# Kernel optimization log

Hardware: AMD Instinct MI355X
Metric: run time of the kernel (lower is better)

The kernel has to match this reference:

```python
import jax, jax.numpy as jnp
import numpy as np

SF, RES, TS = 8192, 40, 1  # sample freq, resolution (orders), time span (s)


def _eofft(inputs, rpm):
    """Engine-order FFT: per-sample zero-pad to length n_i = L + floor((RES*60/rpm_i - TS)*SF),
    FFT along time, keep first SF bins, take magnitude. Implemented as a fully batched
    Bluestein (chirp-z) transform so every sample uses the SAME fixed FFT size M,
    despite different logical FFT lengths n_i.
    """
    B, L, C = inputs.shape            # L == SF (required by the original .view)
    N = SF * TS                       # nonzero signal length after truncation (8192)
    K = SF                            # number of output bins kept (8192)
    M = int(2 ** np.ceil(np.log2(N + K - 1)))  # 16384, fixed batched FFT size

    x = inputs[:, :N, :]              # truncate, [B, N, C]
    pad = jnp.floor((RES * 60.0 / rpm - TS) * SF).astype(jnp.int32)  # [B]
    n = L + pad                       # per-sample DFT length n_i, [B] int32

    # Phases use exact integer m^2 mod 2n (exp(i*pi*q/n) has period 2n in q),
    # so float32 stays accurate even for large m.
    two_n = (2 * n)[:, None]                              # [B,1]
    nf = n.astype(jnp.float32)[:, None]                   # [B,1]

    # a[t] = x[t] * exp(-i*pi*t^2/n)
    t = jnp.arange(N, dtype=jnp.int32)
    a_phase = jnp.pi * ((t * t) % two_n).astype(jnp.float32) / nf      # [B,N]
    a = x.astype(jnp.complex64) * jnp.exp(-1j * a_phase)[:, :, None]   # [B,N,C]
    a = jnp.pad(a, ((0, 0), (0, M - N), (0, 0)))                       # [B,M,C]

    # b[m] = exp(+i*pi*m^2/n), laid out circularly: index m for m<K, index M-m for m=1..N-1
    m = jnp.arange(M, dtype=jnp.int32)
    mm = jnp.minimum(m, M - m)
    b_phase = jnp.pi * ((mm * mm) % two_n).astype(jnp.float32) / nf    # [B,M]
    b = jnp.exp(1j * b_phase)                                          # [B,M]

    # circular convolution via fixed-size FFTs (batched over B and C)
    conv = jnp.fft.ifft(jnp.fft.fft(a, axis=1) * jnp.fft.fft(b, axis=1)[:, :, None], axis=1)

    # X[k] = exp(-i*pi*k^2/n) * conv[k], k = 0..K-1
    k = jnp.arange(K, dtype=jnp.int32)
    k_phase = jnp.pi * ((k * k) % two_n).astype(jnp.float32) / nf      # [B,K]
    X = jnp.exp(-1j * k_phase)[:, :, None] * conv[:, :K, :]            # [B,K,C]
    return jnp.abs(X)                                                  # [B,SF,C] float32


def setup_inputs() -> dict:
    key = jax.random.key(0)
    k1, k2 = jax.random.split(key)
    B, L, C = 64, 8192, 8
    inputs = jax.random.normal(k1, (B, L, C), dtype=jnp.float32)
    rpm = jax.random.uniform(k2, (B,), dtype=jnp.float32, minval=600.0, maxval=2400.0)
    return {"inputs": inputs, "rpm": rpm}


def reference(inputs, rpm):
    return _eofft(inputs, rpm)
```

## Files before the change

kernel.cpp:

```cpp
#include <hip/hip_runtime.h>
#include <hip/hip_fp16.h>
#include <math.h>


static constexpr int Bn = 64;

#define PI_F 3.14159265358979323846f
#define TWO_PI_F 6.28318530717958647692f
#define R2_F 0.70710678118654752f

__device__ __forceinline__ int compute_n(float rpm) {
    return 8192 + (int)floorf((2400.0f / rpm - 1.0f) * 8192.0f);
}
__device__ __forceinline__ float2 cmul(float2 a, float2 b) {
    return make_float2(a.x*b.x - a.y*b.y, a.x*b.y + a.y*b.x);
}
__device__ __forceinline__ float2 cadd(float2 a, float2 b){ return make_float2(a.x+b.x, a.y+b.y); }
__device__ __forceinline__ float2 csub(float2 a, float2 b){ return make_float2(a.x-b.x, a.y-b.y); }
__device__ __forceinline__ float2 shflx1(float2 v) {
    return make_float2(__shfl_xor(v.x, 1, 64), __shfl_xor(v.y, 1, 64));
}
__device__ __forceinline__ int brev7(int x) { return (int)(__brev((unsigned)x) >> 25); }

__device__ __forceinline__ float f2h_bits(float2 a) {
    union { __half2 h; float f; } u;
    u.h = __float22half2_rn(a);
    return u.f;
}
__device__ __forceinline__ float2 h2f_bits(float w) {
    union { float f; __half2 h; } u;
    u.f = w;
    return __half22float2(u.h);
}

#define BF(lo,hi,tw) { float2 _d = csub(lo,hi); lo = cadd(lo,hi); hi = cmul(_d, tw); }
#define BT(lo,hi,tw) { float2 _b = cmul(hi,tw); hi = csub(lo,_b); lo = cadd(lo,_b); }
#define SELC(r,c0,s0,c1,s1) ((r) ? make_float2(c1,s1) : make_float2(c0,s0))
#define IDX(u) ((u) + ((u) >> 4))

__device__ __forceinline__ float2 wtab(const float2* Whi, const float2* Wlo, int m) {
    return cmul(Whi[m >> 7], Wlo[m & 127]);
}

template<bool HZ>
__device__ __forceinline__ void difR(float2 v[8], float2* Lf, int p,
                                     const float2* sWhi) {
    float2 w1 = sWhi[p];
    float2 w2 = cmul(w1, w1);
    float2 w4 = cmul(w2, w2);
    float2 w1b = cmul(w1, make_float2(R2_F,-R2_F));
    float2 w1c = make_float2(w1.y, -w1.x);
    float2 w1d = cmul(w1, make_float2(-R2_F,-R2_F));
    float2 w2i = make_float2(w2.y, -w2.x);
    if (HZ) {
        v[4] = cmul(v[0], w1);
        v[5] = cmul(v[1], w1b);
        v[6] = cmul(v[2], w1c);
        v[7] = cmul(v[3], w1d);
    } else {
        BF(v[0],v[4], w1);
        BF(v[1],v[5], w1b);
        BF(v[2],v[6], w1c);
        BF(v[3],v[7], w1d);
    }
    BF(v[0],v[2], w2);  BF(v[1],v[3], w2i);
    BF(v[4],v[6], w2);  BF(v[5],v[7], w2i);
    BF(v[0],v[1], w4);  BF(v[2],v[3], w4);
    BF(v[4],v[5], w4);  BF(v[6],v[7], w4);
    #pragma unroll
    for (int q = 0; q < 8; ++q) Lf[IDX(p + 16*q)] = v[q];
    int bb = p >> 1, r = p & 1;
    #pragma unroll
    for (int s = 0; s < 8; ++s) v[s] = Lf[IDX(16*bb + r + 2*s)];
    BF(v[0],v[4], SELC(r, 1.f,0.f,                    0.92387953f,-0.38268343f));
    BF(v[1],v[5], SELC(r, 0.70710678f,-0.70710678f,   0.38268343f,-0.92387953f));
    BF(v[2],v[6], SELC(r, 0.f,-1.f,                  -0.38268343f,-0.92387953f));
    BF(v[3],v[7], SELC(r, -0.70710678f,-0.70710678f, -0.92387953f,-0.38268343f));
    BF(v[0],v[2], SELC(r, 1.f,0.f,  0.70710678f,-0.70710678f));
    BF(v[1],v[3], SELC(r, 0.f,-1.f, -0.70710678f,-0.70710678f));
    BF(v[4],v[6], SELC(r, 1.f,0.f,  0.70710678f,-0.70710678f));
    BF(v[5],v[7], SELC(r, 0.f,-1.f, -0.70710678f,-0.70710678f));
    #pragma unroll
    for (int s = 0; s < 8; s += 2) {
        float2 d = csub(v[s], v[s+1]);
        v[s] = cadd(v[s], v[s+1]);
        v[s+1] = r ? make_float2(d.y, -d.x) : d;
    }
    #pragma unroll
    for (int s = 0; s < 8; ++s) {
        float2 o = shflx1(v[s]);
        v[s] = r ? csub(o, v[s]) : cadd(v[s], o);
    }
}

template<bool HOUT>
__device__ __forceinline__ void ditR(float2 v[8], float2* Lf, int p,
                                     const float2* sWhi) {
    int bb = p >> 1, r = p & 1;
    #pragma unroll
    for (int s = 0; s < 8; ++s) {
        float2 o = shflx1(v[s]);
        v[s] = r ? csub(o, v[s]) : cadd(v[s], o);
    }
    #pragma unroll
    for (int s = 0; s < 8; s += 2) {
        float2 bq = v[s+1];
        if (r) bq = make_float2(-bq.y, bq.x);
        v[s+1] = csub(v[s], bq);
        v[s] = cadd(v[s], bq);
    }
    BT(v[0],v[2], SELC(r, 1.f,0.f,  0.70710678f,0.70710678f));
    BT(v[1],v[3], SELC(r, 0.f,1.f, -0.70710678f,0.70710678f));
    BT(v[4],v[6], SELC(r, 1.f,0.f,  0.70710678f,0.70710678f));
    BT(v[5],v[7], SELC(r, 0.f,1.f, -0.70710678f,0.70710678f));
    BT(v[0],v[4], SELC(r, 1.f,0.f,                   0.92387953f,0.38268343f));
    BT(v[1],v[5], SELC(r, 0.70710678f,0.70710678f,   0.38268343f,0.92387953f));
    BT(v[2],v[6], SELC(r, 0.f,1.f,                  -0.38268343f,0.92387953f));
    BT(v[3],v[7], SELC(r, -0.70710678f,0.70710678f, -0.92387953f,0.38268343f));
    #pragma unroll
    for (int s = 0; s < 8; ++s) Lf[IDX(16*bb + r + 2*s)] = v[s];
    #pragma unroll
    for (int q = 0; q < 8; ++q) v[q] = Lf[IDX(p + 16*q)];
    float2 w1 = make_float2(sWhi[p].x, -sWhi[p].y);
    float2 w2 = cmul(w1, w1);
    float2 w4 = cmul(w2, w2);
    float2 w2j = make_float2(-w2.y, w2.x);
    float2 w1b = cmul(w1, make_float2(R2_F, R2_F));
    float2 w1c = make_float2(-w1.y, w1.x);
    float2 w1d = cmul(w1, make_float2(-R2_F, R2_F));
    BT(v[0],v[1], w4); BT(v[2],v[3], w4);
    BT(v[4],v[5], w4); BT(v[6],v[7], w4);
    BT(v[0],v[2], w2);  BT(v[1],v[3], w2j);
    BT(v[4],v[6], w2);  BT(v[5],v[7], w2j);
    if (HOUT) {
        v[0] = cadd(v[0], cmul(v[4], w1));
        v[1] = cadd(v[1], cmul(v[5], w1b));
        v[2] = cadd(v[2], cmul(v[6], w1c));
        v[3] = cadd(v[3], cmul(v[7], w1d));
    } else {
        BT(v[0],v[4], w1);
        BT(v[1],v[5], w1b);
        BT(v[2],v[6], w1c);
        BT(v[3],v[7], w1d);
    }
}

__device__ __forceinline__ void load_tabs(float2* sWhi, float2* sWlo, int tid) {
    if (tid < 128) {
        float sn, cs; __sincosf(PI_F * (float)tid * (1.0f/64.0f), &sn, &cs);
        sWhi[tid] = make_float2(cs, -sn);
    } else if (tid < 256) {
        int m = tid - 128;
        float sn, cs; __sincosf(PI_F * (float)m * (1.0f/8192.0f), &sn, &cs);
        sWlo[m] = make_float2(cs, -sn);
    }
}

__global__ __launch_bounds__(256) void k1b(const float* __restrict__ x,
                                           const float* __restrict__ rpm,
                                           __half2* __restrict__ w1,
                                           __half2* __restrict__ w1c) {
    __shared__ float2 Lw[16 * 137];
    __shared__ float2 chirpT[128];
    __shared__ float2 sWhi[128];
    __shared__ float2 sWlo[128];
    int tid = threadIdx.x;
    int g = tid >> 4, p = tid & 15;
    int bb = p >> 1, r = p & 1;

    load_tabs(sWhi, sWlo, tid);

    if (blockIdx.x < Bn * 8) {
        int b = blockIdx.x >> 3;
        int t1_0 = (blockIdx.x & 7) << 4;
        int n = compute_n(rpm[b]);
        int two_n = 2 * n;
        float inv_n = 1.0f / (float)n;
        #pragma unroll
        for (int i = 0; i < 8; ++i) {
            int l = i * 256 + tid;
            int t2 = l >> 4, c = l & 15;
            int t = (t1_0 + c) + (t2 << 7);
            int mm = min(t, 16384 - t);
            int ph = (mm * mm) % two_n;
            float sn, cs; __sincosf(PI_F * (float)ph * inv_n, &sn, &cs);
            Lw[c * 137 + IDX(t2)] = make_float2(cs, sn);
        }
        __syncthreads();
        float2 v[8];
        #pragma unroll
        for (int q = 0; q < 8; ++q) v[q] = Lw[g * 137 + IDX(p + 16*q)];
        difR<false>(v, Lw + g * 137, p, sWhi);
        __syncthreads();
        {
            int t1 = t1_0 + g;
            int k2base = brev7(16*bb + r);
            float2 cur = wtab(sWhi, sWlo, t1 * k2base);
            float2 w8  = wtab(sWhi, sWlo, 8 * t1);
            #pragma unroll
            for (int e = 0; e < 8; ++e) {
                const int s = ((e & 1) << 2) | (e & 2) | ((e & 4) >> 2);
                Lw[(16*bb + r + 2*s) * 17 + g] = cmul(v[s], cur);
                cur = cmul(cur, w8);
            }
        }
        __syncthreads();
        {
            float4* wb4 = (float4*)(w1c + ((size_t)b << 14) + t1_0);
            #pragma unroll
            for (int i = 0; i < 2; ++i) {
                int l = i * 256 + tid;
                int j = l >> 2, w4 = l & 3;
                float4 val;
                val.x = f2h_bits(Lw[j * 17 + w4*4 + 0]);
                val.y = f2h_bits(Lw[j * 17 + w4*4 + 1]);
                val.z = f2h_bits(Lw[j * 17 + w4*4 + 2]);
                val.w = f2h_bits(Lw[j * 17 + w4*4 + 3]);
                wb4[(size_t)j * 32 + w4] = val;
            }
        }
        return;
    }

    int bid = blockIdx.x - Bn * 8;
    int b = bid >> 6;
    int t1_0 = (bid & 63) << 1;
    int n = compute_n(rpm[b]);
    int two_n = 2 * n;
    float inv_n = 1.0f / (float)n;
    if (tid < 128) {
        int t2 = tid >> 1, t1l = tid & 1;
        int t = t1_0 + t1l + (t2 << 7);
        int ph = (t * t) % two_n;
        float sn, cs; __sincosf(PI_F * (float)ph * inv_n, &sn, &cs);
        chirpT[tid] = make_float2(cs, -sn);
    }
    __syncthreads();
    {
        const float4* xb4 = (const float4*)(x + ((size_t)b << 16));
        int l = tid;
        int t2 = l >> 2, rem = l & 3;
        int t1l = rem >> 1, cp = rem & 1;
        int t = t1_0 + t1l + (t2 << 7);
        float4 xv = xb4[(size_t)t * 2 + cp];
        float2 u = chirpT[t2 * 2 + t1l];
        int c = t1l * 8 + cp * 4;
        Lw[c * 137 + IDX(t2)]       = make_float2(xv.x * u.x, xv.x * u.y);
        Lw[(c + 1) * 137 + IDX(t2)] = make_float2(xv.y * u.x, xv.y * u.y);
        Lw[(c + 2) * 137 + IDX(t2)] = make_float2(xv.z * u.x, xv.z * u.y);
        Lw[(c + 3) * 137 + IDX(t2)] = make_float2(xv.w * u.x, xv.w * u.y);
    }
    __syncthreads();
    float2 v[8];
    #pragma unroll
    for (int q = 0; q < 4; ++q) v[q] = Lw[g * 137 + IDX(p + 16*q)];
    difR<true>(v, Lw + g * 137, p, sWhi);
    __syncthreads();
    {
        int t1 = t1_0 + (g >> 3);
        int k2base = brev7(16*bb + r);
        float2 cur = wtab(sWhi, sWlo, t1 * k2base);
        float2 w8  = wtab(sWhi, sWlo, 8 * t1);
        #pragma unroll
        for (int e = 0; e < 8; ++e) {
            const int s = ((e & 1) << 2) | (e & 2) | ((e & 4) >> 2);
            Lw[(16*bb + r + 2*s) * 17 + g] = cmul(v[s], cur);
            cur = cmul(cur, w8);
        }
    }
    __syncthreads();
    {
        float4* wb4 = (float4*)(w1 + ((size_t)b << 17) + (t1_0 << 3));
        #pragma unroll
        for (int i = 0; i < 2; ++i) {
            int l = i * 256 + tid;
            int j = l >> 2, w4 = l & 3;
            float4 val;
            val.x = f2h_bits(Lw[j * 17 + w4*4 + 0]);
            val.y = f2h_bits(Lw[j * 17 + w4*4 + 1]);
            val.z = f2h_bits(Lw[j * 17 + w4*4 + 2]);
            val.w = f2h_bits(Lw[j * 17 + w4*4 + 3]);
            wb4[(size_t)j * 256 + w4] = val;
        }
    }
}

__global__ __launch_bounds__(256) void k2(const __half2* __restrict__ w1,
                                          const __half2* __restrict__ w1c,
                                          __half2* __restrict__ s2) {
    __shared__ float2 Lw[16 * 137];
    __shared__ float2 Wsc[2 * 137];
    __shared__ float2 sWhi[128];
    __shared__ float2 sWlo[128];
    int tid = threadIdx.x;
    int g = tid >> 4, p = tid & 15;
    int b = blockIdx.x >> 6;
    int j0 = (blockIdx.x & 63) << 1;

    load_tabs(sWhi, sWlo, tid);
    float2 vb[8];
    if (g < 2) {
        const __half2* wc = w1c + ((size_t)b << 14) + ((size_t)(j0 + g) << 7);
        #pragma unroll
        for (int q = 0; q < 8; ++q) vb[q] = __half22float2(wc[p + 16*q]);
    }
    {
        const float4* rb4 = (const float4*)(w1 + ((size_t)b << 17) + ((size_t)j0 << 10));
        #pragma unroll
        for (int i = 0; i < 2; ++i) {
            int l = i * 256 + tid;
            int jl = l >> 8, rem = l & 255, t1 = rem >> 1, ch4 = rem & 1;
            float4 d = rb4[l];
            int c = jl * 8 + ch4 * 4;
            Lw[(c + 0) * 137 + IDX(t1)] = h2f_bits(d.x);
            Lw[(c + 1) * 137 + IDX(t1)] = h2f_bits(d.y);
            Lw[(c + 2) * 137 + IDX(t1)] = h2f_bits(d.z);
            Lw[(c + 3) * 137 + IDX(t1)] = h2f_bits(d.w);
        }
    }
    __syncthreads();
    if (g < 2) {
        difR<false>(vb, Wsc + g * 137, p, sWhi);
        #pragma unroll
        for (int s = 0; s < 8; ++s) Wsc[g * 137 + s * 17 + p] = vb[s];
    }
    float2* Lf = Lw + g * 137;
    float2 v[8];
    #pragma unroll
    for (int q = 0; q < 8; ++q) v[q] = Lf[IDX(p + 16*q)];
    difR<false>(v, Lf, p, sWhi);
    __syncthreads();
    {
        int jl = g >> 3;
        #pragma unroll
        for (int s = 0; s < 8; ++s) v[s] = cmul(v[s], Wsc[jl * 137 + s * 17 + p]);
    }
    ditR<false>(v, Lf, p, sWhi);
    int j = j0 + (g >> 3);
    int k2v = brev7(j);
    __syncthreads();
    {
        float2 cur = wtab(sWhi, sWlo, k2v * p);
        float2 w16 = wtab(sWhi, sWlo, 16 * k2v);
        #pragma unroll
        for (int q = 0; q < 8; ++q) {
            float2 tw = make_float2(cur.x * (1.0f/16384.0f), -cur.y * (1.0f/16384.0f));
            Lw[(p + 16*q) * 17 + g] = cmul(v[q], tw);
            cur = cmul(cur, w16);
        }
    }
    __syncthreads();
    {
        float4* sb4 = (float4*)(s2 + ((size_t)b << 17));
        #pragma unroll
        for (int i = 0; i < 2; ++i) {
            int l = i * 256 + tid;
            int t1 = l >> 2, w4 = l & 3;
            float4 val;
            val.x = f2h_bits(Lw[t1 * 17 + w4*4 + 0]);
            val.y = f2h_bits(Lw[t1 * 17 + w4*4 + 1]);
            val.z = f2h_bits(Lw[t1 * 17 + w4*4 + 2]);
            val.w = f2h_bits(Lw[t1 * 17 + w4*4 + 3]);
            sb4[(size_t)t1 * 256 + (j0 << 1) + w4] = val;
        }
    }
}

__global__ __launch_bounds__(256) void k3(const __half2* __restrict__ s2,
                                          float* __restrict__ outF) {
    __shared__ float2 Lw[16 * 137];
    __shared__ float2 sWhi[128];
    __shared__ float2 sWlo[128];
    int tid = threadIdx.x;
    int g = tid >> 4, p = tid & 15;
    int bb = p >> 1, r = p & 1;
    int b = blockIdx.x >> 6;
    int t1_0 = (blockIdx.x & 63) << 1;

    load_tabs(sWhi, sWlo, tid);
    {
        const float4* rb4 = (const float4*)(s2 + ((size_t)b << 17) + ((size_t)t1_0 << 10));
        #pragma unroll
        for (int i = 0; i < 2; ++i) {
            int l = i * 256 + tid;
            int t1l = l >> 8, rem = l & 255, j = rem >> 1, ch4 = rem & 1;
            float4 d = rb4[l];
            int c = t1l * 8 + ch4 * 4;
            Lw[(c + 0) * 137 + IDX(j)] = h2f_bits(d.x);
            Lw[(c + 1) * 137 + IDX(j)] = h2f_bits(d.y);
            Lw[(c + 2) * 137 + IDX(j)] = h2f_bits(d.z);
            Lw[(c + 3) * 137 + IDX(j)] = h2f_bits(d.w);
        }
    }
    __syncthreads();
    float2 v[8];
    {
        float2* Lf = Lw + g * 137;
        #pragma unroll
        for (int s = 0; s < 8; ++s) v[s] = Lf[IDX(16*bb + r + 2*s)];
        ditR<true>(v, Lf, p, sWhi);
    }
    __syncthreads();
    float* Lsf = (float*)Lw;
    #pragma unroll
    for (int q = 0; q < 4; ++q) {
        float2 z = v[q];
        Lsf[(p + 16*q) * 20 + g] = sqrtf(z.x*z.x + z.y*z.y);
    }
    __syncthreads();
    {
        float4* ob4 = (float4*)(outF + ((size_t)b << 16) + (t1_0 << 3));
        int t2 = tid >> 2, t1l = (tid >> 1) & 1, ch4 = tid & 1;
        int base = t2 * 20 + t1l * 8 + ch4 * 4;
        float4 val = make_float4(Lsf[base], Lsf[base + 1], Lsf[base + 2], Lsf[base + 3]);
        ob4[t2 * 256 + t1l * 2 + ch4] = val;
    }
}

extern "C" void kernel_launch(void* const* d_in, const int* in_sizes, int n_in,
                              void* d_out, int out_size, void* d_ws, size_t ws_size,
                              hipStream_t stream) {
    const float* x   = (const float*)d_in[0];
    const float* rpm = (const float*)d_in[1];
    float* outF = (float*)d_out;
    __half2* w1  = (__half2*)d_ws;
    __half2* s2  = w1 + (size_t)Bn * 131072;
    __half2* w1c = s2 + (size_t)Bn * 131072;

    k1b<<<Bn * 8 + Bn * 64, 256, 0, stream>>>(x, rpm, w1, w1c);
    k2<<<Bn * 64, 256, 0, stream>>>(w1, w1c, s2);
    k3<<<Bn * 64, 256, 0, stream>>>(s2, outF);
}
```

Baseline: 70.37 us.

## Process two column pairs per k3 block with register prefetch; inline chirp in k1b

k3 now handles two consecutive column pairs per block and prefetches the second pair's fp16 data into registers while the first pair is transformed. The grid is halved. This is meant to hide global load latency and amortize twiddle-table setup. In k1b, each thread now computes its own chirp factor with sincos instead of going through a shared table and a barrier. That removes one sync but repeats the sincos for threads that share the same t. The k3 change trades grid parallelism and extra registers for overlap.

```diff
diff --git a/kernel.cpp b/kernel.cpp
--- a/kernel.cpp
+++ b/kernel.cpp
@@ -6,7 +6,6 @@
 static constexpr int Bn = 64;
 
 #define PI_F 3.14159265358979323846f
-#define TWO_PI_F 6.28318530717958647692f
 #define R2_F 0.70710678118654752f
 
 __device__ __forceinline__ int compute_n(float rpm) {
@@ -161,7 +160,6 @@
                                            __half2* __restrict__ w1,
                                            __half2* __restrict__ w1c) {
     __shared__ float2 Lw[16 * 137];
-    __shared__ float2 chirpT[128];
     __shared__ float2 sWhi[128];
     __shared__ float2 sWlo[128];
     int tid = threadIdx.x;
@@ -228,27 +226,21 @@
     int n = compute_n(rpm[b]);
     int two_n = 2 * n;
     float inv_n = 1.0f / (float)n;
-    if (tid < 128) {
-        int t2 = tid >> 1, t1l = tid & 1;
-        int t = t1_0 + t1l + (t2 << 7);
-        int ph = (t * t) % two_n;
-        float sn, cs; __sincosf(PI_F * (float)ph * inv_n, &sn, &cs);
-        chirpT[tid] = make_float2(cs, -sn);
-    }
-    __syncthreads();
     {
         const float4* xb4 = (const float4*)(x + ((size_t)b << 16));
         int l = tid;
         int t2 = l >> 2, rem = l & 3;
         int t1l = rem >> 1, cp = rem & 1;
         int t = t1_0 + t1l + (t2 << 7);
+        int ph = (t * t) % two_n;
+        float sn, cs; __sincosf(PI_F * (float)ph * inv_n, &sn, &cs);
+        float2 uu = make_float2(cs, -sn);
         float4 xv = xb4[(size_t)t * 2 + cp];
-        float2 u = chirpT[t2 * 2 + t1l];
         int c = t1l * 8 + cp * 4;
-        Lw[c * 137 + IDX(t2)]       = make_float2(xv.x * u.x, xv.x * u.y);
-        Lw[(c + 1) * 137 + IDX(t2)] = make_float2(xv.y * u.x, xv.y * u.y);
-        Lw[(c + 2) * 137 + IDX(t2)] = make_float2(xv.z * u.x, xv.z * u.y);
-        Lw[(c + 3) * 137 + IDX(t2)] = make_float2(xv.w * u.x, xv.w * u.y);
+        Lw[c * 137 + IDX(t2)]       = make_float2(xv.x * uu.x, xv.x * uu.y);
+        Lw[(c + 1) * 137 + IDX(t2)] = make_float2(xv.y * uu.x, xv.y * uu.y);
+        Lw[(c + 2) * 137 + IDX(t2)] = make_float2(xv.z * uu.x, xv.z * uu.y);
+        Lw[(c + 3) * 137 + IDX(t2)] = make_float2(xv.w * uu.x, xv.w * uu.y);
     }
     __syncthreads();
     float2 v[8];
@@ -374,46 +366,61 @@
     int tid = threadIdx.x;
     int g = tid >> 4, p = tid & 15;
     int bb = p >> 1, r = p & 1;
-    int b = blockIdx.x >> 6;
-    int t1_0 = (blockIdx.x & 63) << 1;
+    int b = blockIdx.x >> 5;
+    int quad = (blockIdx.x & 31) << 2;
 
     load_tabs(sWhi, sWlo, tid);
-    {
-        const float4* rb4 = (const float4*)(s2 + ((size_t)b << 17) + ((size_t)t1_0 << 10));
+    float4 d0[2], d1[2];
+    {
+        const float4* rb4 = (const float4*)(s2 + ((size_t)b << 17) + ((size_t)quad << 10));
+        d0[0] = rb4[tid];
+        d0[1] = rb4[256 + tid];
+    }
+    #pragma unroll
+    for (int uu = 0; uu < 2; ++uu) {
+        int t1_0 = quad + uu * 2;
+        if (uu == 0) {
+            const float4* rb4n = (const float4*)(s2 + ((size_t)b << 17) + ((size_t)(quad + 2) << 10));
+            d1[0] = rb4n[tid];
+            d1[1] = rb4n[256 + tid];
+        }
+        __syncthreads();
         #pragma unroll
         for (int i = 0; i < 2; ++i) {
             int l = i * 256 + tid;
             int t1l = l >> 8, rem = l & 255, j = rem >> 1, ch4 = rem & 1;
-            float4 d = rb4[l];
+            float4 d = d0[i];
             int c = t1l * 8 + ch4 * 4;
             Lw[(c + 0) * 137 + IDX(j)] = h2f_bits(d.x);
             Lw[(c + 1) * 137 + IDX(j)] = h2f_bits(d.y);
             Lw[(c + 2) * 137 + IDX(j)] = h2f_bits(d.z);
             Lw[(c + 3) * 137 + IDX(j)] = h2f_bits(d.w);
         }
-    }
-    __syncthreads();
-    float2 v[8];
-    {
-        float2* Lf = Lw + g * 137;
-        #pragma unroll
-        for (int s = 0; s < 8; ++s) v[s] = Lf[IDX(16*bb + r + 2*s)];
-        ditR<true>(v, Lf, p, sWhi);
-    }
-    __syncthreads();
-    float* Lsf = (float*)Lw;
-    #pragma unroll
-    for (int q = 0; q < 4; ++q) {
-        float2 z = v[q];
-        Lsf[(p + 16*q) * 20 + g] = sqrtf(z.x*z.x + z.y*z.y);
-    }
-    __syncthreads();
-    {
-        float4* ob4 = (float4*)(outF + ((size_t)b << 16) + (t1_0 << 3));
-        int t2 = tid >> 2, t1l = (tid >> 1) & 1, ch4 = tid & 1;
-        int base = t2 * 20 + t1l * 8 + ch4 * 4;
-        float4 val = make_float4(Lsf[base], Lsf[base + 1], Lsf[base + 2], Lsf[base + 3]);
-        ob4[t2 * 256 + t1l * 2 + ch4] = val;
+        __syncthreads();
+        float2 v[8];
+        {
+            float2* Lf = Lw + g * 137;
+            #pragma unroll
+            for (int s = 0; s < 8; ++s) v[s] = Lf[IDX(16*bb + r + 2*s)];
+            ditR<true>(v, Lf, p, sWhi);
+        }
+        __syncthreads();
+        float* Lsf = (float*)Lw;
+        #pragma unroll
+        for (int q = 0; q < 4; ++q) {
+            float2 z = v[q];
+            Lsf[(p + 16*q) * 20 + g] = sqrtf(z.x*z.x + z.y*z.y);
+        }
+        __syncthreads();
+        {
+            float4* ob4 = (float4*)(outF + ((size_t)b << 16) + (t1_0 << 3));
+            int t2 = tid >> 2, t1l = (tid >> 1) & 1, ch4 = tid & 1;
+            int base = t2 * 20 + t1l * 8 + ch4 * 4;
+            float4 val = make_float4(Lsf[base], Lsf[base + 1], Lsf[base + 2], Lsf[base + 3]);
+            ob4[t2 * 256 + t1l * 2 + ch4] = val;
+        }
+        d0[0] = d1[0];
+        d0[1] = d1[1];
     }
 }
 
@@ -429,5 +436,5 @@
 
     k1b<<<Bn * 8 + Bn * 64, 256, 0, stream>>>(x, rpm, w1, w1c);
     k2<<<Bn * 64, 256, 0, stream>>>(w1, w1c, s2);
-    k3<<<Bn * 64, 256, 0, stream>>>(s2, outF);
-}
+    k3<<<Bn * 32, 256, 0, stream>>>(s2, outF);
+}
```

Result: no change. 71.77 us (+2.0%).
